# Kernel tuning notes

Hardware: AMD Instinct MI355X
Metric: run time of the kernel (lower is better)

Reference implementation:

```python
import jax, jax.numpy as jnp
import numpy as np

NEG_BIG = -1e38

def setup_inputs() -> dict:
    key = jax.random.key(0)
    kq, kk, kv, kwq, kwk = jax.random.split(key, 5)
    B, S, d_model, d_k, d_v = 4, 4096, 256, 64, 64
    return {
        "q": jax.random.normal(kq, (B, S, d_model), dtype=jnp.float32),
        "k": jax.random.normal(kk, (B, S, d_model), dtype=jnp.float32),
        "v": jax.random.normal(kv, (B, S, d_v), dtype=jnp.float32),
        "w_q": jax.random.normal(kwq, (d_k, d_model), dtype=jnp.float32) * 0.01,
        "w_k": jax.random.normal(kwk, (d_k, d_model), dtype=jnp.float32) * 0.01,
    }

def reference(q, k, v, w_q, w_k):
    d_k = w_q.shape[0]
    temperature = jnp.asarray(np.power(d_k, 0.5), dtype=q.dtype)
    # relu-projected Q, K: [B,S,d_k]
    qp = jax.nn.relu(jnp.einsum("bsm,km->bsk", q, w_q))
    kp = jax.nn.relu(jnp.einsum("bsm,km->bsk", k, w_k))
    # scores [B,S,S]
    attn = jnp.einsum("bqd,bkd->bqk", qp, kp) / temperature
    # force column 0 to -1e38 (inline custom mask)
    attn = attn.at[:, :, 0].set(NEG_BIG)
    attn = jax.nn.softmax(attn, axis=2)
    # dropout is identity in eval / p=0
    out = jnp.einsum("bqk,bkd->bqd", attn, v)
    return out
```

## Files before the change

kernel.cpp:

```cpp
#include <hip/hip_runtime.h>

#define B_    4
#define S_    4096
#define DM    256
#define DK    64
#define NROWS (B_ * S_)
#define NPART 4
#define LOG2E 1.4426950408889634f
#define PACK_BIAS 0.0028151295f

typedef __attribute__((ext_vector_type(8))) short bfrag;
typedef __attribute__((ext_vector_type(4))) float ffrag;

__device__ __forceinline__ unsigned bf16_rne_hi(float x) {
    unsigned u = __float_as_uint(x);
    return u + 0x7fffu + ((u >> 16) & 1u);
}
__device__ __forceinline__ unsigned short f2bf(float x) {
    return (unsigned short)(bf16_rne_hi(x) >> 16);
}
__device__ __forceinline__ unsigned pack_bf16x2(float lo, float hi) {
    return (bf16_rne_hi(hi) & 0xffff0000u) | (bf16_rne_hi(lo) >> 16);
}

__device__ __forceinline__ float fast_exp2(float x) {
#if __has_builtin(__builtin_amdgcn_exp2f)
    return __builtin_amdgcn_exp2f(x);
#else
    float r;
    asm("v_exp_f32 %0, %1\n\ts_nop 1" : "=v"(r) : "v"(x));
    return r;
#endif
}

__device__ __forceinline__ unsigned trunc_pack_bf16x2(float lo, float hi) {
    return __builtin_amdgcn_perm(__float_as_uint(hi), __float_as_uint(lo),
                                 0x07060302u);
}

__device__ __forceinline__ void proj_step(
    const float4 xv0, const float4 xv1, const unsigned short* wlds,
    int kf, int m, int quad, ffrag acc[4])
{
    union { bfrag v; unsigned u[4]; } pk;
    pk.u[0] = pack_bf16x2(xv0.x, xv0.y);
    pk.u[1] = pack_bf16x2(xv0.z, xv0.w);
    pk.u[2] = pack_bf16x2(xv1.x, xv1.y);
    pk.u[3] = pack_bf16x2(xv1.z, xv1.w);
#pragma unroll
    for (int dt = 0; dt < 4; ++dt) {
        const bfrag Bf = *(const bfrag*)&wlds[(dt * 16 + m) * 264 + kf * 32 + quad * 8];
        acc[dt] = __builtin_amdgcn_mfma_f32_16x16x32_bf16(pk.v, Bf, acc[dt], 0, 0, 0);
    }
}

__global__ __launch_bounds__(256) void fused_prep(
    const float* __restrict__ q, const float* __restrict__ k,
    const float* __restrict__ v, const float* __restrict__ wq,
    const float* __restrict__ wk, unsigned short* __restrict__ vT,
    unsigned short* __restrict__ qpb, unsigned short* __restrict__ kpb)
{
    __shared__ __align__(16) char smem[64 * 264 * 2];
    const int blk  = blockIdx.x;
    const int tid  = threadIdx.x;
    const int lane = tid & 63, w = tid >> 6;

    if (blk < 256) {
        float (*tile)[65] = (float(*)[65])smem;
        const int b = blk >> 6, s0 = (blk & 63) * 64;
#pragma unroll
        for (int i = 0; i < 16; ++i) {
            const int sl = i * 4 + w;
            tile[sl][lane] = v[(b * S_ + s0 + sl) * DK + lane];
        }
        __syncthreads();
        const int t32 = lane >> 5, pos = lane & 31;
        const int keyl = t32 * 32 + ((pos & 1) ? (pos >> 1) + 16 : (pos >> 1));
#pragma unroll
        for (int i = 0; i < 16; ++i) {
            const int d = i * 4 + w;
            vT[((size_t)(b * 128 + (s0 >> 5) + t32) * 64 + d) * 32 + pos] =
                f2bf(tile[keyl][d]);
        }
    } else {
        unsigned short* wlds = (unsigned short*)smem;
        const int pb = blk - 256;
        const int half = pb >> 8, rblk = pb & 255;
        const float* x;
        const float* wsrc;
        unsigned short* o;
        float scale;
        if (half == 0) { x = q; wsrc = wq; o = qpb; scale = 0.125f * LOG2E; }
        else           { x = k; wsrc = wk; o = kpb; scale = 1.0f; }

        const int m = lane & 15, quad = lane >> 4;
        const int rows0 = rblk * 64 + w * 16;
        const float* xrow = x + (size_t)(rows0 + m) * DM + quad * 8;
        const float4* xf4 = (const float4*)xrow;

        float4 xA[4][2];
#pragma unroll
        for (int t = 0; t < 4; ++t) {
            xA[t][0] = xf4[t * 8];
            xA[t][1] = xf4[t * 8 + 1];
        }

#pragma unroll
        for (int i = 0; i < 16; ++i) {
            const int idx4 = i * 256 + tid;
            const int r = idx4 >> 6, c4 = idx4 & 63;
            const float4 wv = ((const float4*)wsrc)[idx4];
            uint2 pk;
            pk.x = pack_bf16x2(wv.x, wv.y);
            pk.y = pack_bf16x2(wv.z, wv.w);
            *(uint2*)&wlds[r * 264 + c4 * 4] = pk;
        }
        __syncthreads();

        ffrag acc[4];
#pragma unroll
        for (int dt = 0; dt < 4; ++dt) acc[dt] = (ffrag)(0.0f);

        float4 xB[4][2];
#pragma unroll
        for (int kf = 0; kf < 4; ++kf) {
            xB[kf][0] = xf4[(kf + 4) * 8];
            xB[kf][1] = xf4[(kf + 4) * 8 + 1];
            proj_step(xA[kf][0], xA[kf][1], wlds, kf, m, quad, acc);
        }
#pragma unroll
        for (int kf = 0; kf < 4; ++kf)
            proj_step(xB[kf][0], xB[kf][1], wlds, kf + 4, m, quad, acc);

#pragma unroll
        for (int dt = 0; dt < 4; ++dt)
#pragma unroll
            for (int r = 0; r < 4; ++r)
                o[(rows0 + quad * 4 + r) * DK + dt * 16 + m] =
                    f2bf(fmaxf(acc[dt][r], 0.0f) * scale);
    }
}

__global__ __launch_bounds__(256) void attn_mfma(
    const unsigned short* __restrict__ qp, const unsigned short* __restrict__ kp,
    const unsigned short* __restrict__ vT, float* __restrict__ num_part,
    float* __restrict__ den_part)
{
    __shared__ __align__(16) char smem[20480];
    unsigned short* Plds = (unsigned short*)smem;
    float* red0 = (float*)smem;
    float* red1 = (float*)smem + 2560;

    const int lane = threadIdx.x & 63, w = threadIdx.x >> 6;
    const int m = lane & 15, quad = lane >> 4;

    const int flat = blockIdx.x;
    const int wid  = ((flat & 7) << 8) | (flat >> 3);
    const int gy   = wid & 3;
    const int qg   = wid >> 2;

    const int qbase = qg * 32;
    const int b = qg >> 7;
    const int kstart = gy * 1024 + w * 256;

    bfrag qa[2][2];
#pragma unroll
    for (int mt = 0; mt < 2; ++mt)
#pragma unroll
        for (int kf = 0; kf < 2; ++kf)
            qa[mt][kf] = *(const bfrag*)&qp[(qbase + mt * 16 + m) * DK + kf * 32 + quad * 8];

    ffrag oacc[2][4];
    float dacc[2][4];
#pragma unroll
    for (int mt = 0; mt < 2; ++mt) {
#pragma unroll
        for (int dt = 0; dt < 4; ++dt) oacc[mt][dt] = (ffrag)(0.0f);
#pragma unroll
        for (int r = 0; r < 4; ++r) dacc[mt][r] = 0.0f;
    }

    const unsigned short* kptr = kp + ((size_t)b * S_ + kstart + m) * DK + quad * 8;
    const unsigned short* vptr = vT + ((size_t)(b * 128 + (kstart >> 5)) * 64 + m) * 32 + quad * 8;
    unsigned short* Pw = Plds + w * 1280;

    const ffrag cbias = (ffrag)(PACK_BIAS);

    bfrag kbuf[2][2][2], vbuf[2][4];
#pragma unroll
    for (int kt = 0; kt < 2; ++kt)
#pragma unroll
        for (int kf = 0; kf < 2; ++kf)
            kbuf[0][kt][kf] = *(const bfrag*)(kptr + kt * 1024 + kf * 32);
#pragma unroll
    for (int dt = 0; dt < 4; ++dt)
        vbuf[0][dt] = *(const bfrag*)(vptr + dt * 512);

    bfrag pa0, pa1;

#pragma unroll 2
    for (int jj = 0; jj < 8; ++jj) {
        const int p = jj & 1;

        if (jj < 7) {
            const unsigned short* kn = kptr + (jj + 1) * 2048;
#pragma unroll
            for (int kt = 0; kt < 2; ++kt)
#pragma unroll
                for (int kf = 0; kf < 2; ++kf)
                    kbuf[p ^ 1][kt][kf] = *(const bfrag*)(kn + kt * 1024 + kf * 32);
        }

        if (jj > 0) {
#pragma unroll
            for (int dt = 0; dt < 4; ++dt) {
                oacc[0][dt] = __builtin_amdgcn_mfma_f32_16x16x32_bf16(pa0, vbuf[p ^ 1][dt], oacc[0][dt], 0, 0, 0);
                oacc[1][dt] = __builtin_amdgcn_mfma_f32_16x16x32_bf16(pa1, vbuf[p ^ 1][dt], oacc[1][dt], 0, 0, 0);
            }
        }

        if (jj < 7) {
            const unsigned short* vn = vptr + (jj + 1) * 2048;
#pragma unroll
            for (int dt = 0; dt < 4; ++dt)
                vbuf[p ^ 1][dt] = *(const bfrag*)(vn + dt * 512);
        }

        ffrag s[2][2];
#pragma unroll
        for (int mt = 0; mt < 2; ++mt)
#pragma unroll
            for (int kt = 0; kt < 2; ++kt) {
                ffrag t = __builtin_amdgcn_mfma_f32_16x16x32_bf16(qa[mt][0], kbuf[p][kt][0], cbias, 0, 0, 0);
                s[mt][kt] = __builtin_amdgcn_mfma_f32_16x16x32_bf16(qa[mt][1], kbuf[p][kt][1], t, 0, 0, 0);
            }

        const bool mask0 = (jj == 0) && (kstart == 0) && (m == 0);
#pragma unroll
        for (int mt = 0; mt < 2; ++mt)
#pragma unroll
            for (int r = 0; r < 4; ++r) {
                float e0 = fast_exp2(s[mt][0][r]);
                float e1 = fast_exp2(s[mt][1][r]);
                if (mask0) e0 = 0.0f;
                dacc[mt][r] += e0 + e1;
                *(unsigned*)&Pw[(mt * 16 + quad * 4 + r) * 40 + m * 2] =
                    trunc_pack_bf16x2(e0, e1);
            }

        pa0 = *(const bfrag*)&Pw[(m) * 40 + quad * 8];
        pa1 = *(const bfrag*)&Pw[(16 + m) * 40 + quad * 8];
    }
#pragma unroll
    for (int dt = 0; dt < 4; ++dt) {
        oacc[0][dt] = __builtin_amdgcn_mfma_f32_16x16x32_bf16(pa0, vbuf[1][dt], oacc[0][dt], 0, 0, 0);
        oacc[1][dt] = __builtin_amdgcn_mfma_f32_16x16x32_bf16(pa1, vbuf[1][dt], oacc[1][dt], 0, 0, 0);
    }

#pragma unroll
    for (int mt = 0; mt < 2; ++mt)
#pragma unroll
        for (int r = 0; r < 4; ++r) {
            float d = dacc[mt][r];
            d += __shfl_xor(d, 1, 64);
            d += __shfl_xor(d, 2, 64);
            d += __shfl_xor(d, 4, 64);
            d += __shfl_xor(d, 8, 64);
            dacc[mt][r] = d;
        }

    __syncthreads();
    if (w >= 2) {
        float* dst = (w == 2) ? red0 : red1;
#pragma unroll
        for (int mt = 0; mt < 2; ++mt) {
#pragma unroll
            for (int dt = 0; dt < 4; ++dt)
#pragma unroll
                for (int r = 0; r < 4; ++r)
                    dst[((mt * 4 + dt) * 4 + r) * 64 + lane] = oacc[mt][dt][r];
#pragma unroll
            for (int r = 0; r < 4; ++r)
                dst[2048 + (mt * 4 + r) * 64 + lane] = dacc[mt][r];
        }
    }
    __syncthreads();
    if (w < 2) {
        const float* src = (w == 0) ? red0 : red1;
#pragma unroll
        for (int mt = 0; mt < 2; ++mt) {
#pragma unroll
            for (int dt = 0; dt < 4; ++dt)
#pragma unroll
                for (int r = 0; r < 4; ++r)
                    oacc[mt][dt][r] += src[((mt * 4 + dt) * 4 + r) * 64 + lane];
#pragma unroll
            for (int r = 0; r < 4; ++r)
                dacc[mt][r] += src[2048 + (mt * 4 + r) * 64 + lane];
        }
    }
    __syncthreads();
    if (w == 1) {
#pragma unroll
        for (int mt = 0; mt < 2; ++mt) {
#pragma unroll
            for (int dt = 0; dt < 4; ++dt)
#pragma unroll
                for (int r = 0; r < 4; ++r)
                    red0[((mt * 4 + dt) * 4 + r) * 64 + lane] = oacc[mt][dt][r];
#pragma unroll
            for (int r = 0; r < 4; ++r)
                red0[2048 + (mt * 4 + r) * 64 + lane] = dacc[mt][r];
        }
    }
    __syncthreads();
    if (w == 0) {
#pragma unroll
        for (int mt = 0; mt < 2; ++mt) {
#pragma unroll
            for (int dt = 0; dt < 4; ++dt)
#pragma unroll
                for (int r = 0; r < 4; ++r) {
                    const float nv = oacc[mt][dt][r] + red0[((mt * 4 + dt) * 4 + r) * 64 + lane];
                    num_part[(size_t)gy * NROWS * DK +
                             (qbase + mt * 16 + quad * 4 + r) * DK + dt * 16 + m] = nv;
                }
#pragma unroll
            for (int r = 0; r < 4; ++r) {
                const float dv = dacc[mt][r] + red0[2048 + (mt * 4 + r) * 64 + lane];
                if (m == 0)
                    den_part[gy * NROWS + qbase + mt * 16 + quad * 4 + r] = dv;
            }
        }
    }
}

__global__ __launch_bounds__(256) void finalize_kernel(
    const float* __restrict__ num_part, const float* __restrict__ den_part,
    float* __restrict__ out)
{
    const int i4 = blockIdx.x * 256 + threadIdx.x;
    const int row = i4 >> 4;
    const float4 a0 = ((const float4*)num_part)[i4];
    const float4 a1 = ((const float4*)(num_part + (size_t)NROWS * DK))[i4];
    const float4 a2 = ((const float4*)(num_part + (size_t)2 * NROWS * DK))[i4];
    const float4 a3 = ((const float4*)(num_part + (size_t)3 * NROWS * DK))[i4];
    const float inv = 1.0f / (den_part[row] + den_part[NROWS + row] +
                              den_part[2 * NROWS + row] + den_part[3 * NROWS + row]);
    float4 o;
    o.x = (a0.x + a1.x + a2.x + a3.x) * inv;
    o.y = (a0.y + a1.y + a2.y + a3.y) * inv;
    o.z = (a0.z + a1.z + a2.z + a3.z) * inv;
    o.w = (a0.w + a1.w + a2.w + a3.w) * inv;
    ((float4*)out)[i4] = o;
}

extern "C" void kernel_launch(void* const* d_in, const int* in_sizes, int n_in,
                              void* d_out, int out_size, void* d_ws, size_t ws_size,
                              hipStream_t stream)
{
    const float* q  = (const float*)d_in[0];
    const float* k  = (const float*)d_in[1];
    const float* v  = (const float*)d_in[2];
    const float* wq = (const float*)d_in[3];
    const float* wk = (const float*)d_in[4];
    float* out = (float*)d_out;

    char* p = (char*)d_ws;
    unsigned short* qpb = (unsigned short*)p;   p += (size_t)NROWS * DK * 2;
    unsigned short* kpb = (unsigned short*)p;   p += (size_t)NROWS * DK * 2;
    unsigned short* vT  = (unsigned short*)p;   p += (size_t)B_ * DK * S_ * 2;
    float* num_part     = (float*)p;            p += (size_t)NPART * NROWS * DK * 4;
    float* den_part     = (float*)p;

    fused_prep<<<768, 256, 0, stream>>>(q, k, v, wq, wk, vT, qpb, kpb);
    attn_mfma<<<2048, 256, 0, stream>>>(qpb, kpb, vT, num_part, den_part);
    finalize_kernel<<<NROWS * DK / 4 / 256, 256, 0, stream>>>(num_part, den_part, out);
}
```

Baseline: 141.2 us.

## Drop key split across blocks; each block covers full key range and normalizes in-kernel

The attention kernel no longer splits the key dimension into four partitions across blocks. Each block's four waves now each cover 1024 keys, the per-wave partials are reduced in LDS, and the block writes normalized output directly. This removes the partial numerator/denominator buffers and the separate finalize kernel launch, cutting global traffic and one launch. In exchange the grid shrinks from 2048 to 512 blocks, which may leave the GPU underoccupied with fewer blocks per CU to hide latency.

Result: faster. 133.0 us (-5.8%).

```diff
diff --git a/kernel.cpp b/kernel.cpp
--- a/kernel.cpp
+++ b/kernel.cpp
@@ -5,7 +5,6 @@
 #define DM    256
 #define DK    64
 #define NROWS (B_ * S_)
-#define NPART 4
 #define LOG2E 1.4426950408889634f
 #define PACK_BIAS 0.0028151295f
 
@@ -143,8 +142,7 @@
 
 __global__ __launch_bounds__(256) void attn_mfma(
     const unsigned short* __restrict__ qp, const unsigned short* __restrict__ kp,
-    const unsigned short* __restrict__ vT, float* __restrict__ num_part,
-    float* __restrict__ den_part)
+    const unsigned short* __restrict__ vT, float* __restrict__ out)
 {
     __shared__ __align__(16) char smem[20480];
     unsigned short* Plds = (unsigned short*)smem;
@@ -155,13 +153,11 @@
     const int m = lane & 15, quad = lane >> 4;
 
     const int flat = blockIdx.x;
-    const int wid  = ((flat & 7) << 8) | (flat >> 3);
-    const int gy   = wid & 3;
-    const int qg   = wid >> 2;
+    const int qg   = ((flat & 7) << 6) | (flat >> 3);
 
     const int qbase = qg * 32;
     const int b = qg >> 7;
-    const int kstart = gy * 1024 + w * 256;
+    const int kstart = w * 1024;
 
     bfrag qa[2][2];
 #pragma unroll
@@ -199,10 +195,10 @@
     bfrag pa0, pa1;
 
 #pragma unroll 2
-    for (int jj = 0; jj < 8; ++jj) {
+    for (int jj = 0; jj < 32; ++jj) {
         const int p = jj & 1;
 
-        if (jj < 7) {
+        if (jj < 31) {
             const unsigned short* kn = kptr + (jj + 1) * 2048;
 #pragma unroll
             for (int kt = 0; kt < 2; ++kt)
@@ -219,7 +215,7 @@
             }
         }
 
-        if (jj < 7) {
+        if (jj < 31) {
             const unsigned short* vn = vptr + (jj + 1) * 2048;
 #pragma unroll
             for (int dt = 0; dt < 4; ++dt)
@@ -235,7 +231,7 @@
                 s[mt][kt] = __builtin_amdgcn_mfma_f32_16x16x32_bf16(qa[mt][1], kbuf[p][kt][1], t, 0, 0, 0);
             }
 
-        const bool mask0 = (jj == 0) && (kstart == 0) && (m == 0);
+        const bool mask0 = (jj == 0) && (w == 0) && (m == 0);
 #pragma unroll
         for (int mt = 0; mt < 2; ++mt)
 #pragma unroll
@@ -317,42 +313,22 @@
     if (w == 0) {
 #pragma unroll
         for (int mt = 0; mt < 2; ++mt) {
+            float invd[4];
+#pragma unroll
+            for (int r = 0; r < 4; ++r) {
+                const float dv = dacc[mt][r] + red0[2048 + (mt * 4 + r) * 64 + lane];
+                invd[r] = 1.0f / dv;
+            }
 #pragma unroll
             for (int dt = 0; dt < 4; ++dt)
 #pragma unroll
                 for (int r = 0; r < 4; ++r) {
                     const float nv = oacc[mt][dt][r] + red0[((mt * 4 + dt) * 4 + r) * 64 + lane];
-                    num_part[(size_t)gy * NROWS * DK +
-                             (qbase + mt * 16 + quad * 4 + r) * DK + dt * 16 + m] = nv;
+                    out[(size_t)(qbase + mt * 16 + quad * 4 + r) * DK + dt * 16 + m] =
+                        nv * invd[r];
                 }
-#pragma unroll
-            for (int r = 0; r < 4; ++r) {
-                const float dv = dacc[mt][r] + red0[2048 + (mt * 4 + r) * 64 + lane];
-                if (m == 0)
-                    den_part[gy * NROWS + qbase + mt * 16 + quad * 4 + r] = dv;
-            }
-        }
-    }
-}
-
-__global__ __launch_bounds__(256) void finalize_kernel(
-    const float* __restrict__ num_part, const float* __restrict__ den_part,
-    float* __restrict__ out)
-{
-    const int i4 = blockIdx.x * 256 + threadIdx.x;
-    const int row = i4 >> 4;
-    const float4 a0 = ((const float4*)num_part)[i4];
-    const float4 a1 = ((const float4*)(num_part + (size_t)NROWS * DK))[i4];
-    const float4 a2 = ((const float4*)(num_part + (size_t)2 * NROWS * DK))[i4];
-    const float4 a3 = ((const float4*)(num_part + (size_t)3 * NROWS * DK))[i4];
-    const float inv = 1.0f / (den_part[row] + den_part[NROWS + row] +
-                              den_part[2 * NROWS + row] + den_part[3 * NROWS + row]);
-    float4 o;
-    o.x = (a0.x + a1.x + a2.x + a3.x) * inv;
-    o.y = (a0.y + a1.y + a2.y + a3.y) * inv;
-    o.z = (a0.z + a1.z + a2.z + a3.z) * inv;
-    o.w = (a0.w + a1.w + a2.w + a3.w) * inv;
-    ((float4*)out)[i4] = o;
+        }
+    }
 }
 
 extern "C" void kernel_launch(void* const* d_in, const int* in_sizes, int n_in,
@@ -369,11 +345,8 @@
     char* p = (char*)d_ws;
     unsigned short* qpb = (unsigned short*)p;   p += (size_t)NROWS * DK * 2;
     unsigned short* kpb = (unsigned short*)p;   p += (size_t)NROWS * DK * 2;
-    unsigned short* vT  = (unsigned short*)p;   p += (size_t)B_ * DK * S_ * 2;
-    float* num_part     = (float*)p;            p += (size_t)NPART * NROWS * DK * 4;
-    float* den_part     = (float*)p;
+    unsigned short* vT  = (unsigned short*)p;
 
     fused_prep<<<768, 256, 0, stream>>>(q, k, v, wq, wk, vT, qpb, kpb);
-    attn_mfma<<<2048, 256, 0, stream>>>(qpb, kpb, vT, num_part, den_part);
-    finalize_kernel<<<NROWS * DK / 4 / 256, 256, 0, stream>>>(num_part, den_part, out);
-}
+    attn_mfma<<<512, 256, 0, stream>>>(qpb, kpb, vT, out);
+}
```
